# Performance work log

Hardware: AMD Instinct MI355X
Metric: run time of the kernel (lower is better)

The kernel has to match this reference:

```python
import jax, jax.numpy as jnp
import numpy as np

H_DIM = 1024
N_HEADS = 16
SEQ_LEN = 2048
BATCH = 4


def setup_inputs() -> dict:
    key = jax.random.key(0)
    ks = jax.random.split(key, 9)
    s = 1.0 / np.sqrt(H_DIM)
    return {
        "x": jax.random.normal(ks[0], (BATCH, SEQ_LEN, H_DIM), dtype=jnp.float32),
        "Wq": jax.random.normal(ks[1], (H_DIM, H_DIM), dtype=jnp.float32) * s,
        "bq": jax.random.normal(ks[2], (H_DIM,), dtype=jnp.float32) * 0.01,
        "Wk": jax.random.normal(ks[3], (H_DIM, H_DIM), dtype=jnp.float32) * s,
        "bk": jax.random.normal(ks[4], (H_DIM,), dtype=jnp.float32) * 0.01,
        "Wv": jax.random.normal(ks[5], (H_DIM, H_DIM), dtype=jnp.float32) * s,
        "bv": jax.random.normal(ks[6], (H_DIM,), dtype=jnp.float32) * 0.01,
        "Wo": jax.random.normal(ks[7], (H_DIM, H_DIM), dtype=jnp.float32) * s,
        "bo": jax.random.normal(ks[8], (H_DIM,), dtype=jnp.float32) * 0.01,
    }


def reference(x, Wq, bq, Wk, bk, Wv, bv, Wo, bo):
    B, T, C = x.shape
    N = N_HEADS
    D = C // N
    # projections -> [B, N, T, D]
    def split_heads(t):
        return t.reshape(B, T, N, D).transpose(0, 2, 1, 3)
    q = split_heads(x @ Wq + bq)
    k = split_heads(x @ Wk + bk)
    v = split_heads(x @ Wv + bv)
    scale = 1.0 / jnp.sqrt(jnp.asarray(D, dtype=x.dtype))
    logits = jnp.einsum("bntd,bnsd->bnts", q, k) * scale  # [B,N,T,T]
    causal = jnp.tril(jnp.ones((T, T), dtype=bool))
    logits = jnp.where(causal[None, None], logits, jnp.asarray(-jnp.inf, dtype=x.dtype))
    attn = jax.nn.softmax(logits, axis=-1)
    ctx = jnp.einsum("bnts,bnsd->bntd", attn, v)  # [B,N,T,D]
    ctx = ctx.transpose(0, 2, 1, 3).reshape(B, T, C)
    return ctx @ Wo + bo
```

## Files before the change

kernel.cpp:

```cpp
#include <hip/hip_runtime.h>
#include <hip/hip_bf16.h>


typedef __attribute__((ext_vector_type(8))) short bhalf8;
typedef __attribute__((ext_vector_type(4))) float f32x4;

#define BATCH 4
#define SEQ 2048
#define CDIM 1024
#define NHEAD 16
#define HDIM 64
#define MTOT (BATCH * SEQ)
#define QSCALE 0.18033688011112042f

static __device__ inline unsigned short f2bf(float f) {
    unsigned int u = __float_as_uint(f);
    unsigned int r = (u + 0x7fffu + ((u >> 16) & 1u)) >> 16;
    return (unsigned short)r;
}
static __device__ inline float bf2f(unsigned short u) {
    return __uint_as_float(((unsigned int)u) << 16);
}
static __device__ inline f32x4 zero4() {
    f32x4 z = {0.f, 0.f, 0.f, 0.f};
    return z;
}
static __device__ inline f32x4 MFMA(bhalf8 a, bhalf8 b, f32x4 c) {
    return __builtin_amdgcn_mfma_f32_16x16x32_bf16(a, b, c, 0, 0, 0);
}
static __device__ inline void gload16(const void* g, void* l) {
    __builtin_amdgcn_global_load_lds(
        (const __attribute__((address_space(1))) unsigned int*)g,
        (__attribute__((address_space(3))) unsigned int*)l, 16, 0, 0);
}
static __device__ inline unsigned int pkbf16(float lo, float hi) {
    union { __hip_bfloat162 h; unsigned int u; } c;
    c.h = __float22bfloat162_rn(make_float2(lo, hi));
    return c.u;
}

__global__ __launch_bounds__(256) void cast_x_kernel(const float* __restrict__ x,
                                                     short* __restrict__ o, int n8) {
    int i = blockIdx.x * 256 + threadIdx.x;
    if (i >= n8) return;
    const float4* xv = (const float4*)x;
    float4 a = xv[i * 2];
    float4 b = xv[i * 2 + 1];
    bhalf8 r;
    r[0] = (short)f2bf(a.x); r[1] = (short)f2bf(a.y);
    r[2] = (short)f2bf(a.z); r[3] = (short)f2bf(a.w);
    r[4] = (short)f2bf(b.x); r[5] = (short)f2bf(b.y);
    r[6] = (short)f2bf(b.z); r[7] = (short)f2bf(b.w);
    *(bhalf8*)(o + (size_t)i * 8) = r;
}

__global__ __launch_bounds__(256) void wtrans_kernel(const float* __restrict__ W0,
                                                     const float* __restrict__ W1,
                                                     const float* __restrict__ W2,
                                                     const float* __restrict__ W3,
                                                     short* __restrict__ out) {
    __shared__ float t[32][33];
    const float* W = (blockIdx.z == 0) ? W0 : (blockIdx.z == 1) ? W1
                     : (blockIdx.z == 2) ? W2 : W3;
    short* o = out + (size_t)blockIdx.z * CDIM * CDIM;
    int n0 = blockIdx.x * 32, k0 = blockIdx.y * 32;
    int tx = threadIdx.x, ty = threadIdx.y;
    for (int j = 0; j < 4; ++j)
        t[ty + j * 8][tx] = W[(size_t)(k0 + ty + j * 8) * CDIM + n0 + tx];
    __syncthreads();
    for (int j = 0; j < 4; ++j)
        o[(size_t)(n0 + ty + j * 8) * CDIM + k0 + tx] = (short)f2bf(t[tx][ty + j * 8]);
}

template <int MODE, int GN>
__global__ __launch_bounds__(256) void gemm128(const short* __restrict__ A,
                                               const short* __restrict__ Bt,
                                               const float* __restrict__ b0,
                                               const float* __restrict__ b1,
                                               const float* __restrict__ b2,
                                               unsigned short* __restrict__ QKout,
                                               unsigned short* __restrict__ Vout,
                                               float* __restrict__ Fout) {
    __shared__ char lds[32768];
    char* AlB0 = lds;
    char* BlB0 = lds + 16384;

    const int tid = threadIdx.x, lane = tid & 63, w = tid >> 6;
    const int g = lane >> 4, t16 = lane & 15;
    const int wr = w >> 1, wc = w & 1;

    const int f = blockIdx.x;
    const int xcd = f & 7, i = f >> 3;
    const int mt = xcd * 8 + i / GN, nt = i % GN;
    const int tm = mt * 128, tn = nt * 128;
    const int part = tn >> 10;
    const int tnp = tn & 1023;

    const int c0 = tid, c1 = 256 + tid;
    const int r0 = c0 >> 2, r1 = c1 >> 2;
    const int k0c = (c0 & 3) ^ ((r0 >> 1) & 3);
    const int k1c = (c1 & 3) ^ ((r1 >> 1) & 3);
    const short* a0 = A + (size_t)(tm + r0) * 1024 + k0c * 8;
    const short* a1 = A + (size_t)(tm + r1) * 1024 + k1c * 8;
    const short* bp0 = Bt + (size_t)(tn + r0) * 1024 + k0c * 8;
    const short* bp1 = Bt + (size_t)(tn + r1) * 1024 + k1c * 8;

    int aoff[4], boff[4];
#pragma unroll
    for (int mi = 0; mi < 4; ++mi) {
        int row = wr * 64 + mi * 16 + t16;
        aoff[mi] = row * 64 + ((g ^ ((row >> 1) & 3)) << 4);
    }
#pragma unroll
    for (int ni = 0; ni < 4; ++ni) {
        int row = wc * 64 + ni * 16 + t16;
        boff[ni] = row * 64 + ((g ^ ((row >> 1) & 3)) << 4);
    }

    f32x4 acc[4][4];
#pragma unroll
    for (int mi = 0; mi < 4; ++mi)
#pragma unroll
        for (int ni = 0; ni < 4; ++ni) acc[mi][ni] = zero4();

#define STAGE(kt_, bb_)                                                   \
    do {                                                                  \
        int off_ = (kt_) * 32;                                            \
        char* al_ = AlB0 + (bb_) * 8192;                                  \
        char* bl_ = BlB0 + (bb_) * 8192;                                  \
        gload16(a0 + off_, al_ + tid * 16);                               \
        gload16(a1 + off_, al_ + 4096 + tid * 16);                        \
        gload16(bp0 + off_, bl_ + tid * 16);                              \
        gload16(bp1 + off_, bl_ + 4096 + tid * 16);                       \
    } while (0)

    STAGE(0, 0);
    __syncthreads();

#pragma unroll 2
    for (int kt = 0; kt < 32; ++kt) {
        const int buf = kt & 1;
        if (kt + 1 < 32) STAGE(kt + 1, buf ^ 1);
        const char* al = AlB0 + buf * 8192;
        const char* bl = BlB0 + buf * 8192;
        bhalf8 af[4], bfr[4];
#pragma unroll
        for (int mi = 0; mi < 4; ++mi) af[mi] = *(const bhalf8*)(al + aoff[mi]);
#pragma unroll
        for (int ni = 0; ni < 4; ++ni) bfr[ni] = *(const bhalf8*)(bl + boff[ni]);
        __builtin_amdgcn_s_setprio(1);
#pragma unroll
        for (int mi = 0; mi < 4; ++mi)
#pragma unroll
            for (int ni = 0; ni < 4; ++ni)
                acc[mi][ni] = MFMA(af[mi], bfr[ni], acc[mi][ni]);
        __builtin_amdgcn_s_setprio(0);
        __syncthreads();
    }
#undef STAGE

    if (MODE == 0 && part == 2) {
#pragma unroll
        for (int mi = 0; mi < 4; ++mi)
#pragma unroll
            for (int ni = 0; ni < 4; ++ni) {
                int col_l = wc * 64 + ni * 16 + t16;
                float bias = b2[tnp + col_l];
#pragma unroll
                for (int r = 0; r < 4; ++r) {
                    int row_l = wr * 64 + mi * 16 + g * 4 + r;
                    int byte = col_l * 256 + ((row_l * 2) ^ ((col_l & 7) << 4));
                    *(unsigned short*)(lds + byte) = f2bf(acc[mi][ni][r] + bias);
                }
            }
        __syncthreads();
#pragma unroll
        for (int p = 0; p < 8; ++p) {
            int lin = p * 4096 + tid * 16;
            int rv = lin >> 8;
            int inrow = lin & 255;
            int phys = rv * 256 + (inrow ^ ((rv & 7) << 4));
            bhalf8 val = *(const bhalf8*)(lds + phys);
            int n_g = tnp + rv;
            int hh = n_g >> 6, d = n_g & 63;
            int m = tm + (inrow >> 1);
            int bi = m >> 11, t0 = m & 2047;
            *(bhalf8*)(Vout + (((size_t)((bi * NHEAD + hh) * HDIM + d)) << 11) + t0) = val;
        }
    } else {
#pragma unroll
        for (int mi = 0; mi < 4; ++mi)
#pragma unroll
            for (int ni = 0; ni < 4; ++ni) {
                int col_l = wc * 64 + ni * 16 + t16;
                float bias = 0.f;
                if (MODE == 0) bias = (part == 0 ? b0 : b1)[tnp + col_l];
#pragma unroll
                for (int r = 0; r < 4; ++r) {
                    int row_l = wr * 64 + mi * 16 + g * 4 + r;
                    float v = acc[mi][ni][r] + bias;
                    if (MODE == 0 && part == 0) v *= QSCALE;
                    int byte = row_l * 256 + ((col_l * 2) ^ (((row_l >> 2) & 3) << 5));
                    *(unsigned short*)(lds + byte) = f2bf(v);
                }
            }
        __syncthreads();
#pragma unroll
        for (int p = 0; p < 8; ++p) {
            int lin = p * 4096 + tid * 16;
            int row_l = lin >> 8;
            int inrow = lin & 255;
            int phys = row_l * 256 + ((inrow & ~31) ^ (((row_l >> 2) & 3) << 5)) + (inrow & 31);
            bhalf8 val = *(const bhalf8*)(lds + phys);
            int col0 = inrow >> 1;
            int m = tm + row_l;
            if (MODE == 1) {
                int n_g = tn + col0;
                float* op = Fout + (size_t)m * 1024 + n_g;
                float4 o0, o1;
                o0.x = bf2f((unsigned short)val[0]) + b0[n_g + 0];
                o0.y = bf2f((unsigned short)val[1]) + b0[n_g + 1];
                o0.z = bf2f((unsigned short)val[2]) + b0[n_g + 2];
                o0.w = bf2f((unsigned short)val[3]) + b0[n_g + 3];
                o1.x = bf2f((unsigned short)val[4]) + b0[n_g + 4];
                o1.y = bf2f((unsigned short)val[5]) + b0[n_g + 5];
                o1.z = bf2f((unsigned short)val[6]) + b0[n_g + 6];
                o1.w = bf2f((unsigned short)val[7]) + b0[n_g + 7];
                *(float4*)(op) = o0;
                *(float4*)(op + 4) = o1;
            } else {
                int n_g = tnp + col0;
                int bi = m >> 11, t = m & 2047;
                int hh = n_g >> 6, d0 = n_g & 63;
                *(bhalf8*)(QKout +
                           (((size_t)((part * 64 + bi * NHEAD + hh) * SEQ + t)) << 6) + d0) = val;
            }
        }
    }
}

__global__ __launch_bounds__(256) void attn_kernel(const short* __restrict__ Q,
                                                   const short* __restrict__ K,
                                                   const short* __restrict__ V,
                                                   unsigned short* __restrict__ ctx) {
    __shared__ short Kl[2][64 * 64];
    __shared__ short Vl[2][64 * 64];
    __shared__ short Pl[4][16 * 64];

    const int tid = threadIdx.x, lane = tid & 63, w = tid >> 6;
    const int g = lane >> 4, t16 = lane & 15;

    int orig = blockIdx.x;
    int swz = (orig & 7) * 128 + (orig >> 3);
    const int bh = swz >> 4;
    const int sp = swz & 15;

    const short* Qh = Q + ((size_t)bh << 17);
    const short* Kh = K + ((size_t)bh << 17);
    const short* Vh = V + ((size_t)bh << 17);

    int koff[2], voff[2], ldst[2];
#pragma unroll
    for (int it = 0; it < 2; ++it) {
        int c = it * 256 + tid;
        int srow = c >> 3;
        int dc = (c & 7) ^ (srow & 7);
        koff[it] = (srow << 6) + dc * 8;
        voff[it] = (srow << 11) + dc * 8;
        ldst[it] = it * 4096 + w * 1024;
    }

#define STAGE(kv_, bb_)                                                       \
    do {                                                                      \
        gload16(Kh + koff[0] + ((kv_) << 12), (char*)Kl[bb_] + ldst[0]);      \
        gload16(Kh + koff[1] + ((kv_) << 12), (char*)Kl[bb_] + ldst[1]);      \
        gload16(Vh + voff[0] + ((kv_) << 6), (char*)Vl[bb_] + ldst[0]);       \
        gload16(Vh + voff[1] + ((kv_) << 6), (char*)Vl[bb_] + ldst[1]);       \
    } while (0)

    const int b = bh >> 4, hh = bh & 15;
    const int swb = (t16 & 7) << 4;

    int buf = 0;
    STAGE(0, 0);

    for (int ph = 0; ph < 2; ++ph) {
        const int qti = (ph == 0) ? (31 - sp) : sp;
        const int qbase = qti * 64;
        const int ntile = qti + 1;

        bhalf8 qf0, qf1;
        {
            const short* qp = Qh + ((size_t)(qbase + w * 16 + t16) << 6) + g * 8;
            qf0 = *(const bhalf8*)(qp);
            qf1 = *(const bhalf8*)(qp + 32);
        }

        f32x4 acc[4];
#pragma unroll
        for (int i = 0; i < 4; ++i) acc[i] = zero4();
        float l = 0.f;

        __syncthreads();

        for (int kv = 0; kv < ntile; ++kv) {
            if (kv + 1 < ntile) STAGE(kv + 1, buf ^ 1);

            f32x4 lg[4];
            __builtin_amdgcn_s_setprio(1);
#pragma unroll
            for (int cb = 0; cb < 4; ++cb) {
                int s = cb * 16 + t16;
                int sw = (s & 7) << 4;
                const char* rowp = (const char*)Kl[buf] + s * 128;
                bhalf8 k0 = *(const bhalf8*)(rowp + ((g * 16) ^ sw));
                bhalf8 k1 = *(const bhalf8*)(rowp + ((64 + g * 16) ^ sw));
                f32x4 z = zero4();
                z = MFMA(k0, qf0, z);
                z = MFMA(k1, qf1, z);
                lg[cb] = z;
            }
            __builtin_amdgcn_s_setprio(0);

            if (kv == qti) {
                int rowl = w * 16 + t16;
#pragma unroll
                for (int cb = 0; cb < 4; ++cb) {
                    int key0 = cb * 16 + g * 4;
#pragma unroll
                    for (int r = 0; r < 4; ++r)
                        if (key0 + r > rowl) lg[cb][r] = -1e30f;
                }
            }

            {
                float s_ = 0.f;
                int rowbyte = t16 * 128;
#pragma unroll
                for (int cb = 0; cb < 4; ++cb) {
                    float e0 = exp2f(lg[cb][0]);
                    float e1 = exp2f(lg[cb][1]);
                    float e2 = exp2f(lg[cb][2]);
                    float e3 = exp2f(lg[cb][3]);
                    s_ += (e0 + e1) + (e2 + e3);
                    uint2 wv;
                    wv.x = pkbf16(e0, e1);
                    wv.y = pkbf16(e2, e3);
                    int byte = (rowbyte + cb * 32 + g * 8) ^ swb;
                    *(uint2*)((char*)Pl[w] + byte) = wv;
                }
                l += s_;
            }

            __builtin_amdgcn_s_setprio(1);
#pragma unroll
            for (int kk = 0; kk < 2; ++kk) {
                bhalf8 vf[4];
#pragma unroll
                for (int db = 0; db < 4; ++db) {
                    int d = db * 16 + t16;
                    int vbyte = d * 128 + ((kk * 64 + g * 16) ^ ((d & 7) << 4));
                    vf[db] = *(const bhalf8*)((const char*)Vl[buf] + vbyte);
                }
                int abyte = (t16 * 128 + kk * 64 + g * 16) ^ swb;
                bhalf8 pa = *(const bhalf8*)((const char*)Pl[w] + abyte);
#pragma unroll
                for (int db = 0; db < 4; ++db)
                    acc[db] = MFMA(pa, vf[db], acc[db]);
            }
            __builtin_amdgcn_s_setprio(0);

            __syncthreads();
            buf ^= 1;
        }

        if (ph == 0) STAGE(0, buf);

        float lt = l;
        lt += __shfl_xor(lt, 16, 64);
        lt += __shfl_xor(lt, 32, 64);
        float linv = 1.f / lt;
#pragma unroll
        for (int r = 0; r < 4; ++r) {
            float inv = __shfl(linv, g * 4 + r, 64);
            int t = qbase + w * 16 + g * 4 + r;
            size_t rowoff = (((size_t)(b * SEQ + t)) << 10) + hh * 64;
#pragma unroll
            for (int db = 0; db < 4; ++db)
                ctx[rowoff + db * 16 + t16] = f2bf(acc[db][r] * inv);
        }
    }
#undef STAGE
}

extern "C" void kernel_launch(void* const* d_in, const int* in_sizes, int n_in,
                              void* d_out, int out_size, void* d_ws, size_t ws_size,
                              hipStream_t stream) {
    const float* x  = (const float*)d_in[0];
    const float* Wq = (const float*)d_in[1];
    const float* bq = (const float*)d_in[2];
    const float* Wk = (const float*)d_in[3];
    const float* bk = (const float*)d_in[4];
    const float* Wv = (const float*)d_in[5];
    const float* bv = (const float*)d_in[6];
    const float* Wo = (const float*)d_in[7];
    const float* bo = (const float*)d_in[8];

    char* ws = (char*)d_ws;
    short* x16 = (short*)(ws);
    short* Wt  = (short*)(ws + (size_t)16 * 1024 * 1024);
    short* Wot = Wt + (size_t)3 * CDIM * CDIM;
    short* Qb  = (short*)(ws + (size_t)24 * 1024 * 1024);
    short* Vb  = (short*)(ws + (size_t)56 * 1024 * 1024);
    short* Ctx = (short*)(ws + (size_t)72 * 1024 * 1024);

    cast_x_kernel<<<dim3(MTOT * CDIM / 8 / 256), dim3(256), 0, stream>>>(
        x, x16, MTOT * CDIM / 8);
    wtrans_kernel<<<dim3(32, 32, 4), dim3(32, 8), 0, stream>>>(Wq, Wk, Wv, Wo, Wt);

    gemm128<0, 24><<<dim3(1536), dim3(256), 0, stream>>>(
        x16, Wt, bq, bk, bv, (unsigned short*)Qb, (unsigned short*)Vb, nullptr);

    attn_kernel<<<dim3(1024), dim3(256), 0, stream>>>(
        Qb, Qb + (size_t)64 * SEQ * HDIM, Vb, (unsigned short*)Ctx);

    gemm128<1, 8><<<dim3(512), dim3(256), 0, stream>>>(
        Ctx, Wot, bo, nullptr, nullptr, nullptr, nullptr, (float*)d_out);
}
```

Before: 191.9 us.

## Make attention waves independent, loading K/V directly into registers

The attention kernel no longer stages K and V tiles through shared memory with block-wide barriers. Each wave now owns its own 32-row query strip, paired as a long and a short causal strip for balance. Each wave loads K/V fragments straight from global memory into double-buffered registers. Grid size is halved, and each wave handles two 16-row fragments so each K/V load is reused across them. This removes the __syncthreads and LDS staging cost, but the four waves of a block no longer share K/V loads, which raises global/L2 traffic and register pressure.

Measured after the change: 239.6 us. 24.9% more time.

```diff
diff --git a/kernel.cpp b/kernel.cpp
--- a/kernel.cpp
+++ b/kernel.cpp
@@ -243,154 +243,158 @@
                                                    const short* __restrict__ K,
                                                    const short* __restrict__ V,
                                                    unsigned short* __restrict__ ctx) {
-    __shared__ short Kl[2][64 * 64];
-    __shared__ short Vl[2][64 * 64];
-    __shared__ short Pl[4][16 * 64];
+    __shared__ short Pl[4][32 * 64];
 
     const int tid = threadIdx.x, lane = tid & 63, w = tid >> 6;
     const int g = lane >> 4, t16 = lane & 15;
 
     int orig = blockIdx.x;
-    int swz = (orig & 7) * 128 + (orig >> 3);
-    const int bh = swz >> 4;
-    const int sp = swz & 15;
+    int swz = (orig & 7) * 64 + (orig >> 3);
+    const int bh = swz >> 3;
+    const int sp = (swz & 7) * 4 + w;
 
     const short* Qh = Q + ((size_t)bh << 17);
     const short* Kh = K + ((size_t)bh << 17);
     const short* Vh = V + ((size_t)bh << 17);
 
-    int koff[2], voff[2], ldst[2];
-#pragma unroll
-    for (int it = 0; it < 2; ++it) {
-        int c = it * 256 + tid;
-        int srow = c >> 3;
-        int dc = (c & 7) ^ (srow & 7);
-        koff[it] = (srow << 6) + dc * 8;
-        voff[it] = (srow << 11) + dc * 8;
-        ldst[it] = it * 4096 + w * 1024;
-    }
-
-#define STAGE(kv_, bb_)                                                       \
-    do {                                                                      \
-        gload16(Kh + koff[0] + ((kv_) << 12), (char*)Kl[bb_] + ldst[0]);      \
-        gload16(Kh + koff[1] + ((kv_) << 12), (char*)Kl[bb_] + ldst[1]);      \
-        gload16(Vh + voff[0] + ((kv_) << 6), (char*)Vl[bb_] + ldst[0]);       \
-        gload16(Vh + voff[1] + ((kv_) << 6), (char*)Vl[bb_] + ldst[1]);       \
-    } while (0)
-
+    int kel[4], vel[4];
+#pragma unroll
+    for (int cb = 0; cb < 4; ++cb) kel[cb] = (cb * 16 + t16) * 64 + g * 8;
+#pragma unroll
+    for (int db = 0; db < 4; ++db) vel[db] = (db * 16 + t16) * 2048 + g * 8;
+
+    const int s0 = 63 - sp;
+    const int n0 = (s0 >> 1) + 1;
     const int b = bh >> 4, hh = bh & 15;
     const int swb = (t16 & 7) << 4;
-
-    int buf = 0;
-    STAGE(0, 0);
+    char* Pw = (char*)Pl[w];
+
+    bhalf8 ka[8], va[8], kb[8], vb[8];
+
+#define LOADKV(KT, VT, kv_)                                                   \
+    do {                                                                      \
+        const short* kp_ = Kh + ((kv_) << 12);                                \
+        const short* vp_ = Vh + ((kv_) << 6);                                 \
+        _Pragma("unroll") for (int cb = 0; cb < 4; ++cb) {                    \
+            KT[cb * 2]     = *(const bhalf8*)(kp_ + kel[cb]);                 \
+            KT[cb * 2 + 1] = *(const bhalf8*)(kp_ + kel[cb] + 32);            \
+        }                                                                     \
+        _Pragma("unroll") for (int db = 0; db < 4; ++db) {                    \
+            VT[db * 2]     = *(const bhalf8*)(vp_ + vel[db]);                 \
+            VT[db * 2 + 1] = *(const bhalf8*)(vp_ + vel[db] + 32);            \
+        }                                                                     \
+    } while (0)
+
+#define TILE(KT, VT)                                                          \
+    do {                                                                      \
+        f32x4 lg[2][4];                                                       \
+        __builtin_amdgcn_s_setprio(1);                                        \
+        _Pragma("unroll") for (int cb = 0; cb < 4; ++cb)                      \
+            _Pragma("unroll") for (int nf = 0; nf < 2; ++nf) {                \
+                f32x4 z = zero4();                                            \
+                z = MFMA(KT[cb * 2], qf[nf][0], z);                           \
+                z = MFMA(KT[cb * 2 + 1], qf[nf][1], z);                       \
+                lg[nf][cb] = z;                                               \
+            }                                                                 \
+        __builtin_amdgcn_s_setprio(0);                                        \
+        if (kv == nph - 1) {                                                  \
+            _Pragma("unroll") for (int nf = 0; nf < 2; ++nf) {                \
+                int qrow = qb + nf * 16 + t16;                                \
+                _Pragma("unroll") for (int cb = 0; cb < 4; ++cb) {            \
+                    int key0 = kv * 64 + cb * 16 + g * 4;                     \
+                    _Pragma("unroll") for (int r = 0; r < 4; ++r)             \
+                        if (key0 + r > qrow) lg[nf][cb][r] = -1e30f;          \
+                }                                                             \
+            }                                                                 \
+        }                                                                     \
+        _Pragma("unroll") for (int nf = 0; nf < 2; ++nf) {                    \
+            float s_ = 0.f;                                                   \
+            int rowbyte = (nf * 16 + t16) * 128;                              \
+            _Pragma("unroll") for (int cb = 0; cb < 4; ++cb) {                \
+                float e0 = exp2f(lg[nf][cb][0]);                              \
+                float e1 = exp2f(lg[nf][cb][1]);                              \
+                float e2 = exp2f(lg[nf][cb][2]);                              \
+                float e3 = exp2f(lg[nf][cb][3]);                              \
+                s_ += (e0 + e1) + (e2 + e3);                                  \
+                uint2 wv;                                                     \
+                wv.x = pkbf16(e0, e1);                                        \
+                wv.y = pkbf16(e2, e3);                                        \
+                int byte = (rowbyte + cb * 32 + g * 8) ^ swb;                 \
+                *(uint2*)(Pw + byte) = wv;                                    \
+            }                                                                 \
+            l[nf] += s_;                                                      \
+        }                                                                     \
+        __builtin_amdgcn_s_setprio(1);                                        \
+        _Pragma("unroll") for (int kk = 0; kk < 2; ++kk) {                    \
+            _Pragma("unroll") for (int nf = 0; nf < 2; ++nf) {                \
+                int abyte = ((nf * 16 + t16) * 128 + kk * 64 + g * 16) ^ swb; \
+                bhalf8 pa = *(const bhalf8*)(Pw + abyte);                     \
+                _Pragma("unroll") for (int db = 0; db < 4; ++db)              \
+                    acc[nf][db] = MFMA(pa, VT[db * 2 + kk], acc[nf][db]);     \
+            }                                                                 \
+        }                                                                     \
+        __builtin_amdgcn_s_setprio(0);                                        \
+    } while (0)
+
+    LOADKV(ka, va, 0);
+    int j = 0;
 
     for (int ph = 0; ph < 2; ++ph) {
-        const int qti = (ph == 0) ? (31 - sp) : sp;
-        const int qbase = qti * 64;
-        const int ntile = qti + 1;
-
-        bhalf8 qf0, qf1;
-        {
-            const short* qp = Qh + ((size_t)(qbase + w * 16 + t16) << 6) + g * 8;
-            qf0 = *(const bhalf8*)(qp);
-            qf1 = *(const bhalf8*)(qp + 32);
+        const int s = ph ? sp : s0;
+        const int qb = s * 32;
+        const int nph = (s >> 1) + 1;
+
+        bhalf8 qf[2][2];
+#pragma unroll
+        for (int nf = 0; nf < 2; ++nf) {
+            const short* qp = Qh + ((size_t)(qb + nf * 16 + t16) << 6) + g * 8;
+            qf[nf][0] = *(const bhalf8*)(qp);
+            qf[nf][1] = *(const bhalf8*)(qp + 32);
         }
 
-        f32x4 acc[4];
-#pragma unroll
-        for (int i = 0; i < 4; ++i) acc[i] = zero4();
-        float l = 0.f;
-
-        __syncthreads();
-
-        for (int kv = 0; kv < ntile; ++kv) {
-            if (kv + 1 < ntile) STAGE(kv + 1, buf ^ 1);
-
-            f32x4 lg[4];
-            __builtin_amdgcn_s_setprio(1);
-#pragma unroll
-            for (int cb = 0; cb < 4; ++cb) {
-                int s = cb * 16 + t16;
-                int sw = (s & 7) << 4;
-                const char* rowp = (const char*)Kl[buf] + s * 128;
-                bhalf8 k0 = *(const bhalf8*)(rowp + ((g * 16) ^ sw));
-                bhalf8 k1 = *(const bhalf8*)(rowp + ((64 + g * 16) ^ sw));
-                f32x4 z = zero4();
-                z = MFMA(k0, qf0, z);
-                z = MFMA(k1, qf1, z);
-                lg[cb] = z;
+        f32x4 acc[2][4];
+#pragma unroll
+        for (int nf = 0; nf < 2; ++nf)
+#pragma unroll
+            for (int i = 0; i < 4; ++i) acc[nf][i] = zero4();
+        float l[2];
+        l[0] = l[1] = 0.f;
+
+        for (int kv = 0; kv < nph; ++kv, ++j) {
+            int jn = j + 1;
+            int kvn = (jn < n0) ? jn : jn - n0;
+            bool pre = jn < 33;
+            if (j & 1) {
+                if (pre) LOADKV(ka, va, kvn);
+                TILE(kb, vb);
+            } else {
+                if (pre) LOADKV(kb, vb, kvn);
+                TILE(ka, va);
             }
-            __builtin_amdgcn_s_setprio(0);
-
-            if (kv == qti) {
-                int rowl = w * 16 + t16;
-#pragma unroll
-                for (int cb = 0; cb < 4; ++cb) {
-                    int key0 = cb * 16 + g * 4;
-#pragma unroll
-                    for (int r = 0; r < 4; ++r)
-                        if (key0 + r > rowl) lg[cb][r] = -1e30f;
-                }
+        }
+
+        float linv[2];
+#pragma unroll
+        for (int nf = 0; nf < 2; ++nf) {
+            float lt = l[nf];
+            lt += __shfl_xor(lt, 16, 64);
+            lt += __shfl_xor(lt, 32, 64);
+            linv[nf] = 1.f / lt;
+        }
+#pragma unroll
+        for (int nf = 0; nf < 2; ++nf)
+#pragma unroll
+            for (int r = 0; r < 4; ++r) {
+                float inv = __shfl(linv[nf], g * 4 + r, 64);
+                int t = qb + nf * 16 + g * 4 + r;
+                size_t rowoff = (((size_t)(b * SEQ + t)) << 10) + hh * 64;
+#pragma unroll
+                for (int db = 0; db < 4; ++db)
+                    ctx[rowoff + db * 16 + t16] = f2bf(acc[nf][db][r] * inv);
             }
-
-            {
-                float s_ = 0.f;
-                int rowbyte = t16 * 128;
-#pragma unroll
-                for (int cb = 0; cb < 4; ++cb) {
-                    float e0 = exp2f(lg[cb][0]);
-                    float e1 = exp2f(lg[cb][1]);
-                    float e2 = exp2f(lg[cb][2]);
-                    float e3 = exp2f(lg[cb][3]);
-                    s_ += (e0 + e1) + (e2 + e3);
-                    uint2 wv;
-                    wv.x = pkbf16(e0, e1);
-                    wv.y = pkbf16(e2, e3);
-                    int byte = (rowbyte + cb * 32 + g * 8) ^ swb;
-                    *(uint2*)((char*)Pl[w] + byte) = wv;
-                }
-                l += s_;
-            }
-
-            __builtin_amdgcn_s_setprio(1);
-#pragma unroll
-            for (int kk = 0; kk < 2; ++kk) {
-                bhalf8 vf[4];
-#pragma unroll
-                for (int db = 0; db < 4; ++db) {
-                    int d = db * 16 + t16;
-                    int vbyte = d * 128 + ((kk * 64 + g * 16) ^ ((d & 7) << 4));
-                    vf[db] = *(const bhalf8*)((const char*)Vl[buf] + vbyte);
-                }
-                int abyte = (t16 * 128 + kk * 64 + g * 16) ^ swb;
-                bhalf8 pa = *(const bhalf8*)((const char*)Pl[w] + abyte);
-#pragma unroll
-                for (int db = 0; db < 4; ++db)
-                    acc[db] = MFMA(pa, vf[db], acc[db]);
-            }
-            __builtin_amdgcn_s_setprio(0);
-
-            __syncthreads();
-            buf ^= 1;
-        }
-
-        if (ph == 0) STAGE(0, buf);
-
-        float lt = l;
-        lt += __shfl_xor(lt, 16, 64);
-        lt += __shfl_xor(lt, 32, 64);
-        float linv = 1.f / lt;
-#pragma unroll
-        for (int r = 0; r < 4; ++r) {
-            float inv = __shfl(linv, g * 4 + r, 64);
-            int t = qbase + w * 16 + g * 4 + r;
-            size_t rowoff = (((size_t)(b * SEQ + t)) << 10) + hh * 64;
-#pragma unroll
-            for (int db = 0; db < 4; ++db)
-                ctx[rowoff + db * 16 + t16] = f2bf(acc[db][r] * inv);
-        }
     }
-#undef STAGE
+#undef TILE
+#undef LOADKV
 }
 
 extern "C" void kernel_launch(void* const* d_in, const int* in_sizes, int n_in,
@@ -421,7 +425,7 @@
     gemm128<0, 24><<<dim3(1536), dim3(256), 0, stream>>>(
         x16, Wt, bq, bk, bv, (unsigned short*)Qb, (unsigned short*)Vb, nullptr);
 
-    attn_kernel<<<dim3(1024), dim3(256), 0, stream>>>(
+    attn_kernel<<<dim3(512), dim3(256), 0, stream>>>(
         Qb, Qb + (size_t)64 * SEQ * HDIM, Vb, (unsigned short*)Ctx);
 
     gemm128<1, 8><<<dim3(512), dim3(256), 0, stream>>>(
```
